# Kernel optimization log

Measured on AMD Instinct MI355X. Metric: run time of the kernel, lower is better.

## Reference

```python
import jax, jax.numpy as jnp
import numpy as np

# ---- static config (mirrors cfg) ----
B, N, K = 2, 8192, 40
FIRST_DL = 0.03
CONV_RADIUS = 2.5
DEFORM_RADIUS = 5.0
ARCH = ['simple', 'resnetb', 'resnetb_strided', 'resnetb', 'resnetb_strided', 'resnetb', 'nearest_upsample']
SENTINEL = N  # out-of-range support index (torch code uses N_spts_total; here per-batch padded slot count)
GRID = 4096   # voxel hash multiplier; coords stay < GRID for pts in [0,1], dl >= 0.06


def _ball_query_one(q, s, qmask, smask, radius):
    """Radius ball-query: K nearest supports within radius. q:[N,3] s:[M,3]."""
    d2 = jnp.sum((q[:, None, :] - s[None, :, :]) ** 2, axis=-1)          # [N,M]
    d2 = jnp.where(smask[None, :] & (d2 <= radius * radius), d2, jnp.inf)
    vals, idx = jax.lax.top_k(-d2, K)                                     # [N,K]
    idx = jnp.where(jnp.isfinite(vals) & qmask[:, None], idx, SENTINEL)
    return idx.astype(jnp.int32)


ball_query = jax.vmap(_ball_query_one, in_axes=(0, 0, 0, 0, None))


def _grid_subsample_one(pts, mask, dl):
    """Voxel-grid subsampling with unweighted average (padded to N rows)."""
    INT_MAX = jnp.iinfo(jnp.int32).max
    c = jnp.floor(pts / dl).astype(jnp.int32)                             # nonneg for pts in [0,1]
    key_v = (c[:, 0] * GRID + c[:, 1]) * GRID + c[:, 2]
    key_v = jnp.where(mask, key_v, INT_MAX)
    order = jnp.argsort(key_v)
    sk = key_v[order]
    sp = pts[order]
    new = jnp.concatenate([jnp.ones((1,), bool), sk[1:] != sk[:-1]])
    seg = jnp.cumsum(new) - 1                                             # segment id per sorted point
    sums = jax.ops.segment_sum(sp, seg, num_segments=N)                   # [N,3]
    cnt = jax.ops.segment_sum(jnp.ones((N,), pts.dtype), seg, num_segments=N)
    segkey = jax.ops.segment_max(sk, seg, num_segments=N)
    valid = (cnt > 0) & (segkey != INT_MAX)                               # invalid pads sort last
    means = jnp.where(valid[:, None], sums / jnp.maximum(cnt, 1.0)[:, None], 0.0)
    return means, valid, jnp.sum(valid).astype(jnp.int32)


grid_subsample = jax.vmap(_grid_subsample_one, in_axes=(0, 0, None))


def setup_inputs() -> dict:
    key = jax.random.key(0)
    pts = jax.random.uniform(key, (B, N, 3), dtype=jnp.float32)
    return {"pts": pts}


def reference(pts):
    pmask = jnp.ones((B, N), bool)
    lengths = jnp.full((B,), N, jnp.int32)
    points = pts
    r_normal = FIRST_DL * CONV_RADIUS
    layer_blocks = []
    out_points, out_neigh, out_pool, out_up, out_len = [], [], [], [], []
    for bi, block in enumerate(ARCH):
        if 'global' in block or 'upsample' in block:
            break
        if not ('pool' in block or 'strided' in block):
            layer_blocks.append(block)
            if bi < len(ARCH) - 1 and 'upsample' not in ARCH[bi + 1]:
                continue
        if layer_blocks:
            if any('deformable' in b for b in layer_blocks[:-1]):
                r = r_normal * DEFORM_RADIUS / CONV_RADIUS
            else:
                r = r_normal
            conv_i = ball_query(points, points, pmask, pmask, r)
        else:
            conv_i = jnp.full((B, N, K), SENTINEL, jnp.int32)
        if 'pool' in block or 'strided' in block:
            dl = 2 * r_normal / CONV_RADIUS
            pool_p, pool_m, pool_len = grid_subsample(points, pmask, dl)
            r = r_normal * DEFORM_RADIUS / CONV_RADIUS if 'deformable' in block else r_normal
            pool_i = ball_query(pool_p, points, pool_m, pmask, r)
            up_i = ball_query(points, pool_p, pmask, pool_m, 2 * r)
        else:
            pool_i = jnp.full((B, N, K), SENTINEL, jnp.int32)
            up_i = jnp.full((B, N, K), SENTINEL, jnp.int32)
            pool_p = jnp.zeros((B, N, 3), points.dtype)
            pool_m = jnp.zeros((B, N), bool)
            pool_len = jnp.zeros((B,), jnp.int32)
        out_points.append(points)
        out_neigh.append(conv_i)
        out_pool.append(pool_i)
        out_up.append(up_i)
        out_len.append(lengths)
        points, pmask, lengths = pool_p, pool_m, pool_len
        r_normal *= 2
        layer_blocks = []
    return (jnp.stack(out_points),   # [L,B,N,3] padded points per layer
            jnp.stack(out_neigh),    # [L,B,N,K] conv neighbor indices
            jnp.stack(out_pool),     # [L,B,N,K] pooling indices
            jnp.stack(out_up),       # [L,B,N,K] upsampling indices
            jnp.stack(out_len))      # [L,B]     valid lengths
```

## Files before the change

### kernel.cpp

```cpp
#include <hip/hip_runtime.h>

#define BB   2
#define NN   8192
#define KNN  40
#define SENT 8192
#define G0   17
#define G1   9
#define G0_3 (G0*G0*G0)
#define G1_3 (G1*G1*G1)

#define GA   13
#define GB   6
#define GC   3
#define GA_3 (GA*GA*GA)
#define GB_3 (GB*GB*GB)
#define GC_3 (GC*GC*GC)

typedef unsigned long long ull;
typedef unsigned int       u32;
typedef unsigned short     u16;

__device__ __forceinline__ float sqdist(float qx, float qy, float qz,
                                        float sx, float sy, float sz) {
    float dx = __fsub_rn(qx, sx);
    float dy = __fsub_rn(qy, sy);
    float dz = __fsub_rn(qz, sz);
    return __fadd_rn(__fadd_rn(__fmul_rn(dx, dx), __fmul_rn(dy, dy)),
                     __fmul_rn(dz, dz));
}

__device__ __forceinline__ int cell1(float p, float Gf, int G) {
    int c = (int)floorf(__fmul_rn(p, Gf));
    return min(max(c, 0), G - 1);
}
__device__ __forceinline__ int vcell1(float p, float dlf, int G) {
    int c = (int)floorf(__fdiv_rn(p, dlf));
    return min(max(c, 0), G - 1);
}

__device__ __forceinline__ ull shfl_u64(ull x, int src) {
    int lo = __shfl((int)(u32)x, src);
    int hi = __shfl((int)(u32)(x >> 32), src);
    return ((ull)(u32)hi << 32) | (ull)(u32)lo;
}
__device__ __forceinline__ ull shflxor_u64(ull x, int m) {
    int lo = __shfl_xor((int)(u32)x, m);
    int hi = __shfl_xor((int)(u32)(x >> 32), m);
    return ((ull)(u32)hi << 32) | (ull)(u32)lo;
}

__global__ void prep_kernel(const float* __restrict__ pts, float* __restrict__ dout) {
    const size_t PN = (size_t)BB * NN * 3;
    const size_t IN = (size_t)BB * NN * KNN;
    float* out_points0 = dout;
    float* out_pool2   = dout + 3 * PN + 3 * IN + 2 * IN;
    float* out_up2     = dout + 3 * PN + 6 * IN + 2 * IN;
    float* out_len     = dout + 3 * PN + 9 * IN;
    int i = blockIdx.x * 256 + threadIdx.x;
    if (i < (int)PN) out_points0[i] = pts[i];
    if (i < (int)IN) {
        out_pool2[i] = (float)SENT;
        out_up2[i]   = (float)SENT;
    }
    if (i == 0) { out_len[0] = (float)NN; out_len[1] = (float)NN; }
}

__global__ __launch_bounds__(1024) void csr_build(
    const float* __restrict__ pts, const int* __restrict__ len_ptr, int len_const,
    int G, int G3, int* __restrict__ off, float4* __restrict__ lst4,
    float dlfv, int Gv, int G3v, int* __restrict__ offv, int* __restrict__ rankv,
    int* __restrict__ lstv, int* __restrict__ lenv_dev, float* __restrict__ lenv_out_f) {
    __shared__ int scnt[GA_3];
    __shared__ int soff[GA_3];
    __shared__ int svcnt[G0_3];
    __shared__ int svoff[G0_3];
    __shared__ int wsum[16];
    int b = blockIdx.x;
    int t = threadIdx.x;
    int len = len_ptr ? len_ptr[b] : len_const;
    const float* pb = pts + (size_t)b * NN * 3;
    float Gf = (float)G;
    bool dosub = Gv > 0;
    for (int v = t; v < G3; v += 1024) scnt[v] = 0;
    if (dosub) for (int v = t; v < G3v; v += 1024) svcnt[v] = 0;
    __syncthreads();
    for (int i = t; i < len; i += 1024) {
        float px = pb[i * 3], py = pb[i * 3 + 1], pz = pb[i * 3 + 2];
        int c = (cell1(px, Gf, G) * G + cell1(py, Gf, G)) * G + cell1(pz, Gf, G);
        atomicAdd(&scnt[c], 1);
        if (dosub) {
            int cv = (vcell1(px, dlfv, Gv) * Gv + vcell1(py, dlfv, Gv)) * Gv
                     + vcell1(pz, dlfv, Gv);
            atomicAdd(&svcnt[cv], 1);
        }
    }
    __syncthreads();
    int lane = t & 63, wid = t >> 6;
    {
        int per = (G3 + 1023) >> 10;
        int start = t * per, end = min(start + per, G3);
        if (start > G3) start = G3;
        int csum = 0;
        for (int v = start; v < end; ++v) csum += scnt[v];
        int inc = csum;
        for (int d = 1; d < 64; d <<= 1) {
            int u = __shfl_up(inc, d);
            if (lane >= d) inc += u;
        }
        if (lane == 63) wsum[wid] = inc;
        __syncthreads();
        if (t < 16) {
            int wv = wsum[t];
            for (int d = 1; d < 16; d <<= 1) {
                int u = __shfl_up(wv, d);
                if (t >= d) wv += u;
            }
            wsum[t] = wv;
        }
        __syncthreads();
        int excl = inc - csum + (wid ? wsum[wid - 1] : 0);
        int run = excl;
        int* offb = off + (size_t)b * (G3 + 1);
        for (int v = start; v < end; ++v) {
            soff[v] = run;
            offb[v] = run;
            run += scnt[v];
        }
        if (t == 0) offb[G3] = len;
    }
    __syncthreads();
    if (dosub) {
        int per = (G3v + 1023) >> 10;
        int start = t * per, end = min(start + per, G3v);
        if (start > G3v) start = G3v;
        int ce = 0, co = 0;
        for (int v = start; v < end; ++v) { ce += svcnt[v]; co += (svcnt[v] > 0); }
        int pack = (ce << 14) | co;
        int inc = pack;
        for (int d = 1; d < 64; d <<= 1) {
            int u = __shfl_up(inc, d);
            if (lane >= d) inc += u;
        }
        if (lane == 63) wsum[wid] = inc;
        __syncthreads();
        if (t < 16) {
            int wv = wsum[t];
            for (int d = 1; d < 16; d <<= 1) {
                int u = __shfl_up(wv, d);
                if (t >= d) wv += u;
            }
            wsum[t] = wv;
        }
        __syncthreads();
        int excl = inc - pack + (wid ? wsum[wid - 1] : 0);
        int rune = excl >> 14;
        int runo = excl & 16383;
        int total = wsum[15] & 16383;
        int* offvb  = offv  + (size_t)b * (G3v + 1);
        int* rankvb = rankv + (size_t)b * G3v;
        for (int v = start; v < end; ++v) {
            svoff[v]  = rune;
            offvb[v]  = rune;
            rankvb[v] = runo;
            rune += svcnt[v];
            runo += (svcnt[v] > 0);
        }
        if (t == 0) {
            offvb[G3v] = len;
            lenv_dev[b] = total;
            lenv_out_f[b] = (float)total;
        }
    }
    __syncthreads();
    for (int v = t; v < G3; v += 1024) scnt[v] = 0;
    if (dosub) for (int v = t; v < G3v; v += 1024) svcnt[v] = 0;
    __syncthreads();
    float4* lst4b = lst4 + (size_t)b * NN;
    int* lstvb = dosub ? (lstv + (size_t)b * NN) : nullptr;
    for (int i = t; i < len; i += 1024) {
        float px = pb[i * 3], py = pb[i * 3 + 1], pz = pb[i * 3 + 2];
        int c = (cell1(px, Gf, G) * G + cell1(py, Gf, G)) * G + cell1(pz, Gf, G);
        int pos = soff[c] + atomicAdd(&scnt[c], 1);
        lst4b[pos] = make_float4(px, py, pz, __int_as_float(i));
        if (dosub) {
            int cv = (vcell1(px, dlfv, Gv) * Gv + vcell1(py, dlfv, Gv)) * Gv
                     + vcell1(pz, dlfv, Gv);
            int posv = svoff[cv] + atomicAdd(&svcnt[cv], 1);
            lstvb[posv] = i;
        }
    }
}

__global__ __launch_bounds__(256) void sub_means(
    const float* __restrict__ pts, const int* __restrict__ offg,
    const int* __restrict__ rankg, const int* __restrict__ lst,
    const int* __restrict__ len_dev, int G3, float* __restrict__ out_pts) {
    int b = blockIdx.y;
    int i = blockIdx.x * 256 + threadIdx.x;
    const float* pb = pts + (size_t)b * NN * 3;
    const int* offb  = offg + (size_t)b * (G3 + 1);
    const int* lstb  = lst + (size_t)b * NN;
    if (i < G3) {
        int s = offb[i], e = offb[i + 1];
        int cn = e - s;
        if (cn > 0) {
            float sx = 0.f, sy = 0.f, sz = 0.f;
            int last = -1;
            for (int k = 0; k < cn; ++k) {
                int m = 0x7FFFFFFF;
                for (int j = s; j < e; ++j) {
                    int idx = lstb[j];
                    if (idx > last && idx < m) m = idx;
                }
                sx = __fadd_rn(sx, pb[m * 3]);
                sy = __fadd_rn(sy, pb[m * 3 + 1]);
                sz = __fadd_rn(sz, pb[m * 3 + 2]);
                last = m;
            }
            float rinv = __frcp_rn((float)cn);
            int rk = rankg[(size_t)b * G3 + i];
            float* op = out_pts + ((size_t)b * NN + rk) * 3;
            op[0] = __fmul_rn(sx, rinv);
            op[1] = __fmul_rn(sy, rinv);
            op[2] = __fmul_rn(sz, rinv);
        }
    }
    int total = len_dev[b];
    if (i >= total && i < NN) {
        float* op = out_pts + ((size_t)b * NN + i) * 3;
        op[0] = 0.f; op[1] = 0.f; op[2] = 0.f;
    }
}

struct BqArgs {
    const float* q; const int* qlp; int qlc;
    const float4* lst; const int* off;
    int G; int G3; float r2; float* out;
};

__global__ __launch_bounds__(256) void bq_wave4(BqArgs pA, BqArgs pB,
                                                BqArgs pC, BqArgs pD) {
    const ull INITK = ~0ull;
    __shared__ ull wlds[4][512];
    int z = blockIdx.z;
    const float* qpts   = z == 0 ? pA.q   : (z == 1 ? pB.q   : (z == 2 ? pC.q   : pD.q));
    const int* qlen_ptr = z == 0 ? pA.qlp : (z == 1 ? pB.qlp : (z == 2 ? pC.qlp : pD.qlp));
    int qlen_const      = z == 0 ? pA.qlc : (z == 1 ? pB.qlc : (z == 2 ? pC.qlc : pD.qlc));
    const float4* lst   = z == 0 ? pA.lst : (z == 1 ? pB.lst : (z == 2 ? pC.lst : pD.lst));
    const int* off      = z == 0 ? pA.off : (z == 1 ? pB.off : (z == 2 ? pC.off : pD.off));
    int G               = z == 0 ? pA.G   : (z == 1 ? pB.G   : (z == 2 ? pC.G   : pD.G));
    int G3              = z == 0 ? pA.G3  : (z == 1 ? pB.G3  : (z == 2 ? pC.G3  : pD.G3));
    float r2            = z == 0 ? pA.r2  : (z == 1 ? pB.r2  : (z == 2 ? pC.r2  : pD.r2));
    float* out          = z == 0 ? pA.out : (z == 1 ? pB.out : (z == 2 ? pC.out : pD.out));

    int t = threadIdx.x;
    int lane = t & 63;
    ull* wl = wlds[t >> 6];
    int b = blockIdx.y;
    int qi = blockIdx.x * 4 + (t >> 6);
    int qlen = qlen_ptr ? qlen_ptr[b] : qlen_const;
    float* op = out + ((size_t)b * NN + qi) * KNN;
    if (qi >= qlen) {
        if (lane < KNN) op[lane] = (float)SENT;
        return;
    }
    const float* qp = qpts + ((size_t)b * NN + qi) * 3;
    float qx = qp[0], qy = qp[1], qz = qp[2];
    float Gf = (float)G;
    int cx = cell1(qx, Gf, G), cy = cell1(qy, Gf, G), cz = cell1(qz, Gf, G);
    const int* offb = off + (size_t)b * (G3 + 1);
    const float4* lstb = lst + (size_t)b * NN;

    int cnt = 0, cst = 0;
    if (lane < 27) {
        int dz = lane % 3 - 1, dy = (lane / 3) % 3 - 1, dxx = lane / 9 - 1;
        int x = cx + dxx, y = cy + dy, zz = cz + dz;
        bool ok = ((unsigned)x < (unsigned)G) & ((unsigned)y < (unsigned)G)
                                              & ((unsigned)zz < (unsigned)G);
        int c = ok ? (x * G + y) * G + zz : 0;
        int s = ok ? offb[c] : 0;
        int e = ok ? offb[c + 1] : 0;
        cnt = e - s;
        cst = s;
    }
    int incl = cnt;
#pragma unroll
    for (int d_ = 1; d_ < 64; d_ <<= 1) {
        int u = __shfl_up(incl, d_);
        if (lane >= d_) incl += u;
    }
    int excl = incl - cnt;
    int T = __shfl(incl, 63);

    ull res = INITK;
    bool have_res = false;
    for (int r0 = 0; r0 < T; r0 += 512) {
        ull c0 = INITK, c1 = INITK, c2 = INITK, c3 = INITK,
            c4 = INITK, c5 = INITK, c6 = INITK, c7 = INITK;
#define FILL(S, CS) if (r0 + (S) * 64 < T) {                                   \
            int g = r0 + (S) * 64 + lane;                                      \
            bool gok = g < T;                                                  \
            int gc = gok ? g : (T - 1);                                        \
            int d = 0;                                                         \
            if (__shfl(excl, d | 16) <= gc) d |= 16;                           \
            if (__shfl(excl, d | 8)  <= gc) d |= 8;                            \
            if (__shfl(excl, d | 4)  <= gc) d |= 4;                            \
            if (__shfl(excl, d | 2)  <= gc) d |= 2;                            \
            if (__shfl(excl, d | 1)  <= gc) d |= 1;                            \
            int st = __shfl(cst, d), eg = __shfl(excl, d);                     \
            float4 f = lstb[st + (gc - eg)];                                   \
            float d2 = sqdist(qx, qy, qz, f.x, f.y, f.z);                      \
            if (gok && d2 <= r2)                                               \
                CS = (((ull)__float_as_uint(d2)) << 13)                        \
                     | (ull)(u32)__float_as_int(f.w);                          \
        }
        FILL(0, c0) FILL(1, c1) FILL(2, c2) FILL(3, c3)
        FILL(4, c4) FILL(5, c5) FILL(6, c6) FILL(7, c7)
#undef FILL
#define CE(A, B) { ull lo_ = (A < B) ? A : B; ull hi_ = (A < B) ? B : A; A = lo_; B = hi_; }
        CE(c0,c1) CE(c2,c3) CE(c4,c5) CE(c6,c7)
        CE(c0,c2) CE(c1,c3) CE(c4,c6) CE(c5,c7)
        CE(c1,c2) CE(c5,c6)
        CE(c0,c4) CE(c1,c5) CE(c2,c6) CE(c3,c7)
        CE(c2,c4) CE(c3,c5)
        CE(c1,c2) CE(c3,c4) CE(c5,c6)
#undef CE
        int m = (c0 != INITK) + (c1 != INITK) + (c2 != INITK) + (c3 != INITK)
              + (c4 != INITK) + (c5 != INITK) + (c6 != INITK) + (c7 != INITK);
        int incm = m;
#pragma unroll
        for (int d_ = 1; d_ < 64; d_ <<= 1) {
            int u = __shfl_up(incm, d_);
            if (lane >= d_) incm += u;
        }
        int base = incm - m;
        int M = __shfl(incm, 63);
        asm volatile("s_waitcnt lgkmcnt(0)" ::: "memory");
        __builtin_amdgcn_sched_barrier(0);
        if (m > 0) {
            wl[base] = c0;
            if (m > 1) wl[base + 1] = c1;
            if (m > 2) wl[base + 2] = c2;
            if (m > 3) wl[base + 3] = c3;
            if (m > 4) wl[base + 4] = c4;
            if (m > 5) wl[base + 5] = c5;
            if (m > 6) wl[base + 6] = c6;
            if (m > 7) wl[base + 7] = c7;
        }
        asm volatile("s_waitcnt lgkmcnt(0)" ::: "memory");
        __builtin_amdgcn_sched_barrier(0);
        int npass = (M + 63) >> 6;
        for (int p = 0; p < npass; ++p) {
            int D = p * 64 + lane;
            ull key = (D < M) ? wl[D] : INITK;
            int mc = M - p * 64;
#pragma unroll
            for (int k = 2; k <= 32; k <<= 1) {
#pragma unroll
                for (int jj = k >> 1; jj > 0; jj >>= 1) {
                    ull other = shflxor_u64(key, jj);
                    bool up = ((lane & k) == 0);
                    bool lowlane = ((lane & jj) == 0);
                    bool takeMin = (lowlane == up);
                    bool lt = key < other;
                    key = (takeMin == lt) ? key : other;
                }
            }
            if (mc > 32) {
#pragma unroll
                for (int jj = 32; jj > 0; jj >>= 1) {
                    ull other = shflxor_u64(key, jj);
                    bool lowlane = ((lane & jj) == 0);
                    bool lt = key < other;
                    key = (lowlane == lt) ? key : other;
                }
            }
            if (!have_res) {
                res = key;
                have_res = true;
            } else {
                ull rb = shfl_u64(key, 63 - lane);
                ull lo_ = (res < rb) ? res : rb;
#pragma unroll
                for (int jj = 32; jj > 0; jj >>= 1) {
                    ull other = shflxor_u64(lo_, jj);
                    bool lowlane = ((lane & jj) == 0);
                    bool lt = lo_ < other;
                    lo_ = (lowlane == lt) ? lo_ : other;
                }
                res = lo_;
            }
        }
    }
    if (lane < KNN)
        op[lane] = (res == INITK) ? (float)SENT : (float)(int)(res & 0x1FFFu);
}

extern "C" void kernel_launch(void* const* d_in, const int* in_sizes, int n_in,
                              void* d_out, int out_size, void* d_ws, size_t ws_size,
                              hipStream_t stream) {
    const float* pts = (const float*)d_in[0];
    float* dout = (float*)d_out;
    const size_t PN = (size_t)BB * NN * 3;
    const size_t IN = (size_t)BB * NN * KNN;
    float* out_points = dout;
    float* out_neigh  = dout + 3 * PN;
    float* out_pool   = out_neigh + 3 * IN;
    float* out_up     = out_pool + 3 * IN;
    float* out_len    = out_up + 3 * IN;
    float* pts1 = out_points + PN;
    float* pts2 = out_points + 2 * PN;

    float4* lst4A = (float4*)d_ws;
    float4* lst4B = lst4A + (size_t)BB * NN;
    float4* lst4C = lst4B + (size_t)BB * NN;
    int*   len1  = (int*)(lst4C + (size_t)BB * NN);
    int*   len2  = len1 + BB;
    int*   offV0 = len2 + BB;
    int*   rnk0  = offV0 + (size_t)BB * (G0_3 + 1);
    int*   lstV0 = rnk0 + (size_t)BB * G0_3;
    int*   offV1 = lstV0 + (size_t)BB * NN;
    int*   rnk1  = offV1 + (size_t)BB * (G1_3 + 1);
    int*   lstV1 = rnk1 + (size_t)BB * G1_3;
    int*   offA  = lstV1 + (size_t)BB * NN;
    int*   offB  = offA + (size_t)BB * (GA_3 + 1);
    int*   offC  = offB + (size_t)BB * (GB_3 + 1);

    double r_normal = 0.03 * 2.5;
    double r0 = r_normal;
    double dl0 = 2.0 * r_normal / 2.5;
    float r2_0   = (float)(r0 * r0);
    float r2_up0 = (float)((2.0 * r0) * (2.0 * r0));
    float dlf0   = (float)dl0;
    r_normal *= 2.0;
    double r1 = r_normal;
    double dl1 = 2.0 * r_normal / 2.5;
    float r2_1   = (float)(r1 * r1);
    float r2_up1 = (float)((2.0 * r1) * (2.0 * r1));
    float dlf1   = (float)dl1;
    r_normal *= 2.0;
    float r2_2 = (float)(r_normal * r_normal);

    BqArgs conv0 = { pts,  nullptr, NN, lst4A, offA, GA, GA_3, r2_0,   out_neigh + 0 * IN };
    BqArgs pool0 = { pts1, len1,    0,  lst4A, offA, GA, GA_3, r2_0,   out_pool  + 0 * IN };
    BqArgs up0   = { pts,  nullptr, NN, lst4B, offB, GB, GB_3, r2_up0, out_up    + 0 * IN };
    BqArgs conv1 = { pts1, len1,    0,  lst4B, offB, GB, GB_3, r2_1,   out_neigh + 1 * IN };
    BqArgs pool1 = { pts2, len2,    0,  lst4B, offB, GB, GB_3, r2_1,   out_pool  + 1 * IN };
    BqArgs up1   = { pts1, len1,    0,  lst4C, offC, GC, GC_3, r2_up1, out_up    + 1 * IN };
    BqArgs conv2 = { pts2, len2,    0,  lst4C, offC, GC, GC_3, r2_2,   out_neigh + 2 * IN };

    dim3 qgrid3(NN / 4, BB, 3);
    dim3 qgrid4(NN / 4, BB, 4);
    dim3 mgrid(NN / 256, BB);

    prep_kernel<<<(int)((IN + 255) / 256), 256, 0, stream>>>(pts, dout);
    csr_build<<<BB, 1024, 0, stream>>>(pts, nullptr, NN, GA, GA_3, offA, lst4A,
                                       dlf0, G0, G0_3, offV0, rnk0, lstV0,
                                       len1, out_len + 2);
    sub_means<<<mgrid, 256, 0, stream>>>(pts, offV0, rnk0, lstV0, len1, G0_3, pts1);
    csr_build<<<BB, 1024, 0, stream>>>(pts1, len1, 0, GB, GB_3, offB, lst4B,
                                       dlf1, G1, G1_3, offV1, rnk1, lstV1,
                                       len2, out_len + 4);
    sub_means<<<mgrid, 256, 0, stream>>>(pts1, offV1, rnk1, lstV1, len2, G1_3, pts2);
    csr_build<<<BB, 1024, 0, stream>>>(pts2, len2, 0, GC, GC_3, offC, lst4C,
                                       0.f, 0, 0, nullptr, nullptr, nullptr,
                                       nullptr, nullptr);
    bq_wave4<<<qgrid3, 256, 0, stream>>>(conv0, pool0, up0, up0);
    bq_wave4<<<qgrid4, 256, 0, stream>>>(conv1, pool1, up1, conv2);
}
```

Measured before the change: 189.3 us.

## Fuse subsample means into ball-query launches and skip unneeded bitonic stages

Drops the standalone sub_means kernel and folds it into a fused ball-query kernel as extra z-slices. Each ball query is rescheduled to launch as soon as its CSR grid exists, so conv0 runs alongside the first means and pool0/up0/conv1 run alongside the second. This cuts one launch and lets independent work overlap instead of waiting on serial dependencies. Separately, the per-pass bitonic sort now skips stages larger than the candidate count needs. The cost is more branching in the sort and a kernel that mixes very different block workloads.

```diff
diff --git a/kernel.cpp b/kernel.cpp
--- a/kernel.cpp
+++ b/kernel.cpp
@@ -191,67 +191,69 @@
     }
 }
 
-__global__ __launch_bounds__(256) void sub_means(
-    const float* __restrict__ pts, const int* __restrict__ offg,
-    const int* __restrict__ rankg, const int* __restrict__ lst,
-    const int* __restrict__ len_dev, int G3, float* __restrict__ out_pts) {
-    int b = blockIdx.y;
-    int i = blockIdx.x * 256 + threadIdx.x;
-    const float* pb = pts + (size_t)b * NN * 3;
-    const int* offb  = offg + (size_t)b * (G3 + 1);
-    const int* lstb  = lst + (size_t)b * NN;
-    if (i < G3) {
-        int s = offb[i], e = offb[i + 1];
-        int cn = e - s;
-        if (cn > 0) {
-            float sx = 0.f, sy = 0.f, sz = 0.f;
-            int last = -1;
-            for (int k = 0; k < cn; ++k) {
-                int m = 0x7FFFFFFF;
-                for (int j = s; j < e; ++j) {
-                    int idx = lstb[j];
-                    if (idx > last && idx < m) m = idx;
-                }
-                sx = __fadd_rn(sx, pb[m * 3]);
-                sy = __fadd_rn(sy, pb[m * 3 + 1]);
-                sz = __fadd_rn(sz, pb[m * 3 + 2]);
-                last = m;
-            }
-            float rinv = __frcp_rn((float)cn);
-            int rk = rankg[(size_t)b * G3 + i];
-            float* op = out_pts + ((size_t)b * NN + rk) * 3;
-            op[0] = __fmul_rn(sx, rinv);
-            op[1] = __fmul_rn(sy, rinv);
-            op[2] = __fmul_rn(sz, rinv);
-        }
-    }
-    int total = len_dev[b];
-    if (i >= total && i < NN) {
-        float* op = out_pts + ((size_t)b * NN + i) * 3;
-        op[0] = 0.f; op[1] = 0.f; op[2] = 0.f;
-    }
-}
-
 struct BqArgs {
     const float* q; const int* qlp; int qlc;
     const float4* lst; const int* off;
     int G; int G3; float r2; float* out;
 };
-
-__global__ __launch_bounds__(256) void bq_wave4(BqArgs pA, BqArgs pB,
-                                                BqArgs pC, BqArgs pD) {
+struct MeansArgs {
+    const float* pts; const int* off; const int* rnk; const int* lst;
+    const int* len_dev; int G3; float* out;
+};
+
+__global__ __launch_bounds__(256) void bq_fused(BqArgs pA, BqArgs pB, BqArgs pC,
+                                                MeansArgs pM, int nbq) {
     const ull INITK = ~0ull;
     __shared__ ull wlds[4][512];
     int z = blockIdx.z;
-    const float* qpts   = z == 0 ? pA.q   : (z == 1 ? pB.q   : (z == 2 ? pC.q   : pD.q));
-    const int* qlen_ptr = z == 0 ? pA.qlp : (z == 1 ? pB.qlp : (z == 2 ? pC.qlp : pD.qlp));
-    int qlen_const      = z == 0 ? pA.qlc : (z == 1 ? pB.qlc : (z == 2 ? pC.qlc : pD.qlc));
-    const float4* lst   = z == 0 ? pA.lst : (z == 1 ? pB.lst : (z == 2 ? pC.lst : pD.lst));
-    const int* off      = z == 0 ? pA.off : (z == 1 ? pB.off : (z == 2 ? pC.off : pD.off));
-    int G               = z == 0 ? pA.G   : (z == 1 ? pB.G   : (z == 2 ? pC.G   : pD.G));
-    int G3              = z == 0 ? pA.G3  : (z == 1 ? pB.G3  : (z == 2 ? pC.G3  : pD.G3));
-    float r2            = z == 0 ? pA.r2  : (z == 1 ? pB.r2  : (z == 2 ? pC.r2  : pD.r2));
-    float* out          = z == 0 ? pA.out : (z == 1 ? pB.out : (z == 2 ? pC.out : pD.out));
+    if (z >= nbq) {
+        int b = blockIdx.y;
+        int i = blockIdx.x * 256 + threadIdx.x;
+        if (i >= NN) return;
+        const float* pb = pM.pts + (size_t)b * NN * 3;
+        const int* offb = pM.off + (size_t)b * (pM.G3 + 1);
+        const int* lstb = pM.lst + (size_t)b * NN;
+        if (i < pM.G3) {
+            int s = offb[i], e = offb[i + 1];
+            int cn = e - s;
+            if (cn > 0) {
+                float sx = 0.f, sy = 0.f, sz = 0.f;
+                int last = -1;
+                for (int k = 0; k < cn; ++k) {
+                    int m = 0x7FFFFFFF;
+                    for (int j = s; j < e; ++j) {
+                        int idx = lstb[j];
+                        if (idx > last && idx < m) m = idx;
+                    }
+                    sx = __fadd_rn(sx, pb[m * 3]);
+                    sy = __fadd_rn(sy, pb[m * 3 + 1]);
+                    sz = __fadd_rn(sz, pb[m * 3 + 2]);
+                    last = m;
+                }
+                float rinv = __frcp_rn((float)cn);
+                int rk = pM.rnk[(size_t)b * pM.G3 + i];
+                float* op = pM.out + ((size_t)b * NN + rk) * 3;
+                op[0] = __fmul_rn(sx, rinv);
+                op[1] = __fmul_rn(sy, rinv);
+                op[2] = __fmul_rn(sz, rinv);
+            }
+        }
+        int total = pM.len_dev[blockIdx.y];
+        if (i >= total) {
+            float* op = pM.out + ((size_t)blockIdx.y * NN + i) * 3;
+            op[0] = 0.f; op[1] = 0.f; op[2] = 0.f;
+        }
+        return;
+    }
+    const float* qpts   = z == 0 ? pA.q   : (z == 1 ? pB.q   : pC.q);
+    const int* qlen_ptr = z == 0 ? pA.qlp : (z == 1 ? pB.qlp : pC.qlp);
+    int qlen_const      = z == 0 ? pA.qlc : (z == 1 ? pB.qlc : pC.qlc);
+    const float4* lst   = z == 0 ? pA.lst : (z == 1 ? pB.lst : pC.lst);
+    const int* off      = z == 0 ? pA.off : (z == 1 ? pB.off : pC.off);
+    int G               = z == 0 ? pA.G   : (z == 1 ? pB.G   : pC.G);
+    int G3              = z == 0 ? pA.G3  : (z == 1 ? pB.G3  : pC.G3);
+    float r2            = z == 0 ? pA.r2  : (z == 1 ? pB.r2  : pC.r2);
+    float* out          = z == 0 ? pA.out : (z == 1 ? pB.out : pC.out);
 
     int t = threadIdx.x;
     int lane = t & 63;
@@ -354,27 +356,22 @@
             int D = p * 64 + lane;
             ull key = (D < M) ? wl[D] : INITK;
             int mc = M - p * 64;
-#pragma unroll
-            for (int k = 2; k <= 32; k <<= 1) {
-#pragma unroll
-                for (int jj = k >> 1; jj > 0; jj >>= 1) {
-                    ull other = shflxor_u64(key, jj);
-                    bool up = ((lane & k) == 0);
-                    bool lowlane = ((lane & jj) == 0);
-                    bool takeMin = (lowlane == up);
-                    bool lt = key < other;
-                    key = (takeMin == lt) ? key : other;
-                }
-            }
-            if (mc > 32) {
-#pragma unroll
-                for (int jj = 32; jj > 0; jj >>= 1) {
-                    ull other = shflxor_u64(key, jj);
-                    bool lowlane = ((lane & jj) == 0);
-                    bool lt = key < other;
-                    key = (lowlane == lt) ? key : other;
-                }
-            }
+#define BSTAGE(K) { _Pragma("unroll")                                          \
+            for (int jj = (K) >> 1; jj > 0; jj >>= 1) {                        \
+                ull other = shflxor_u64(key, jj);                              \
+                bool up = ((lane & (K)) == 0);                                 \
+                bool lowlane = ((lane & jj) == 0);                             \
+                bool takeMin = (lowlane == up);                                \
+                bool lt = key < other;                                         \
+                key = (takeMin == lt) ? key : other;                           \
+            } }
+            if (mc > 1)  BSTAGE(2)
+            if (mc > 2)  BSTAGE(4)
+            if (mc > 4)  BSTAGE(8)
+            if (mc > 8)  BSTAGE(16)
+            if (mc > 16) BSTAGE(32)
+            if (mc > 32) BSTAGE(64)
+#undef BSTAGE
             if (!have_res) {
                 res = key;
                 have_res = true;
@@ -448,23 +445,24 @@
     BqArgs pool1 = { pts2, len2,    0,  lst4B, offB, GB, GB_3, r2_1,   out_pool  + 1 * IN };
     BqArgs up1   = { pts1, len1,    0,  lst4C, offC, GC, GC_3, r2_up1, out_up    + 1 * IN };
     BqArgs conv2 = { pts2, len2,    0,  lst4C, offC, GC, GC_3, r2_2,   out_neigh + 2 * IN };
-
-    dim3 qgrid3(NN / 4, BB, 3);
-    dim3 qgrid4(NN / 4, BB, 4);
-    dim3 mgrid(NN / 256, BB);
+    MeansArgs means0 = { pts,  offV0, rnk0, lstV0, len1, G0_3, pts1 };
+    MeansArgs means1 = { pts1, offV1, rnk1, lstV1, len2, G1_3, pts2 };
+
+    dim3 gD1(NN / 4, BB, 2);
+    dim3 gD2(NN / 4, BB, 4);
+    dim3 gD3(NN / 4, BB, 3);
 
     prep_kernel<<<(int)((IN + 255) / 256), 256, 0, stream>>>(pts, dout);
     csr_build<<<BB, 1024, 0, stream>>>(pts, nullptr, NN, GA, GA_3, offA, lst4A,
                                        dlf0, G0, G0_3, offV0, rnk0, lstV0,
                                        len1, out_len + 2);
-    sub_means<<<mgrid, 256, 0, stream>>>(pts, offV0, rnk0, lstV0, len1, G0_3, pts1);
+    bq_fused<<<gD1, 256, 0, stream>>>(conv0, conv0, conv0, means0, 1);
     csr_build<<<BB, 1024, 0, stream>>>(pts1, len1, 0, GB, GB_3, offB, lst4B,
                                        dlf1, G1, G1_3, offV1, rnk1, lstV1,
                                        len2, out_len + 4);
-    sub_means<<<mgrid, 256, 0, stream>>>(pts1, offV1, rnk1, lstV1, len2, G1_3, pts2);
+    bq_fused<<<gD2, 256, 0, stream>>>(pool0, up0, conv1, means1, 3);
     csr_build<<<BB, 1024, 0, stream>>>(pts2, len2, 0, GC, GC_3, offC, lst4C,
                                        0.f, 0, 0, nullptr, nullptr, nullptr,
                                        nullptr, nullptr);
-    bq_wave4<<<qgrid3, 256, 0, stream>>>(conv0, pool0, up0, up0);
-    bq_wave4<<<qgrid4, 256, 0, stream>>>(conv1, pool1, up1, conv2);
-}
+    bq_fused<<<gD3, 256, 0, stream>>>(pool1, up1, conv2, means1, 3);
+}
```

Measured after the change: 179.5 us (median of 2 runs). -5.2%, faster.
